# Kernel optimization log

Hardware: AMD Instinct MI355X
Metric: run time of the kernel (lower is better)

## Reference

```python
import jax, jax.numpy as jnp
import numpy as np

N_SRC = 100_000   # hetero[s].num_nodes
N_DST = 100_000   # hetero[d].num_nodes
E     = 800_000   # edge_index.size(1)
D_SRC = 256       # node_dims['src']
D_DST = 256       # node_dims['dst']
D_REL = 128       # d_rel


def setup_inputs() -> dict:
    key = jax.random.key(0)
    ks = jax.random.split(key, 6)
    x_src = jax.random.normal(ks[0], (N_SRC, D_SRC), jnp.float32)
    x_dst = jax.random.normal(ks[1], (N_DST, D_DST), jnp.float32)
    # nn.Linear(d_in, d_rel, bias=False) weights, stored transposed as [d_in, d_rel]
    W_src = jax.random.normal(ks[2], (D_SRC, D_REL), jnp.float32) / np.sqrt(D_SRC).astype(np.float32)
    W_dst = jax.random.normal(ks[3], (D_DST, D_REL), jnp.float32) / np.sqrt(D_DST).astype(np.float32)
    edge_src = jax.random.randint(ks[4], (E,), 0, N_SRC, jnp.int32)  # edge_index[0]
    edge_dst = jax.random.randint(ks[5], (E,), 0, N_DST, jnp.int32)  # edge_index[1]
    return {"x_src": x_src, "x_dst": x_dst, "W_src": W_src, "W_dst": W_dst,
            "edge_src": edge_src, "edge_dst": edge_dst}


def reference(x_src, x_dst, W_src, W_dst, edge_src, edge_dst):
    # Per-type linear projection (bias-free), as in self.proj[nt](feats)
    p_src = x_src @ W_src            # [N_src, d_rel]
    p_dst = x_dst @ W_dst            # projected per module, unused by this edge type
    del p_dst

    # Degree of each destination (A.sum(dim=1)), clamped to >= 1.
    deg = jax.ops.segment_sum(jnp.ones((E,), jnp.float32), edge_dst,
                              num_segments=N_DST)
    deg = jnp.maximum(deg, 1.0)      # [N_dst]

    # Degree-normalized SpMM: sum of source features per destination / deg.
    # (coalescing duplicate edges sums their unit values; segment_sum matches.)
    agg = jax.ops.segment_sum(p_src[edge_src], edge_dst,
                              num_segments=N_DST)            # [N_dst, d_rel]
    dst = agg / deg[:, None]

    # rel_embs[et] = {'dst': dst, 'src_in': x_proj[s], 'deg_dst': deg}
    return dst, p_src, deg
```

## Files before the change

### kernel.cpp

```cpp
#include <hip/hip_runtime.h>
#include <hip/hip_bf16.h>

#define D_SRC 256
#define D_REL 128

typedef __bf16 bf16x8 __attribute__((ext_vector_type(8)));
typedef float f32x4 __attribute__((ext_vector_type(4)));

__global__ void zero_kernel(int* __restrict__ p, int n) {
    int i = blockIdx.x * 256 + threadIdx.x;
    if (i < n) p[i] = 0;
}

__global__ __launch_bounds__(64) void prep_w_kernel(const float* __restrict__ W,
                                                    bf16x8* __restrict__ Wt) {
    int c = blockIdx.x;
    int ks = c >> 3, n = c & 7;
    int lane = threadIdx.x;
    int col = n * 16 + (lane & 15);
    int k0 = ks * 32 + (lane >> 4) * 8;
    bf16x8 v;
#pragma unroll
    for (int j = 0; j < 8; ++j) v[j] = (__bf16)W[(size_t)(k0 + j) * D_REL + col];
    Wt[c * 64 + lane] = v;
}

__global__ __launch_bounds__(512) void proj_mfma_kernel(
    const float* __restrict__ x, const f32x4* __restrict__ Wt,
    float* __restrict__ out, unsigned short* __restrict__ out_bf, int M) {
    __shared__ f32x4 blds[4096];
    int tid = threadIdx.x;
#pragma unroll
    for (int i = 0; i < 8; ++i) blds[tid + i * 512] = Wt[tid + i * 512];

    int wave = tid >> 6, lane = tid & 63;
    int row = blockIdx.x * 128 + wave * 16 + (lane & 15);
    int rowc = min(row, M - 1);
    int kb = lane >> 4;

    f32x4 acc[8];
#pragma unroll
    for (int n = 0; n < 8; ++n) acc[n] = (f32x4)(0.f);

    __syncthreads();

    const float* xr = x + (size_t)rowc * D_SRC + kb * 8;
    const bf16x8* b8 = (const bf16x8*)blds;
#pragma unroll
    for (int ks = 0; ks < 8; ++ks) {
        f32x4 a0 = *(const f32x4*)(xr + ks * 32);
        f32x4 a1 = *(const f32x4*)(xr + ks * 32 + 4);
        bf16x8 af;
        af[0] = (__bf16)a0[0]; af[1] = (__bf16)a0[1];
        af[2] = (__bf16)a0[2]; af[3] = (__bf16)a0[3];
        af[4] = (__bf16)a1[0]; af[5] = (__bf16)a1[1];
        af[6] = (__bf16)a1[2]; af[7] = (__bf16)a1[3];
#pragma unroll
        for (int n = 0; n < 8; ++n) {
            bf16x8 bf = b8[ks * 512 + n * 64 + lane];
            acc[n] = __builtin_amdgcn_mfma_f32_16x16x32_bf16(af, bf, acc[n], 0, 0, 0);
        }
    }

    int orow0 = blockIdx.x * 128 + wave * 16 + (lane >> 4) * 4;
    int ocol = lane & 15;
#pragma unroll
    for (int reg = 0; reg < 4; ++reg) {
        int r = orow0 + reg;
        if (r < M) {
            float* o = out + (size_t)r * D_REL + ocol;
            unsigned short* ob = out_bf + (size_t)r * D_REL + ocol;
#pragma unroll
            for (int n = 0; n < 8; ++n) {
                float v = acc[n][reg];
                o[n * 16] = v;
                ob[n * 16] = (unsigned short)(__bfloat16_as_ushort(__float2bfloat16(v)));
            }
        }
    }
}

__global__ void count_kernel(const int* __restrict__ edge_dst, int* __restrict__ deg_i,
                             int* __restrict__ pos_arr, int E) {
    int e = blockIdx.x * 256 + threadIdx.x;
    if (e < E) pos_arr[e] = atomicAdd(&deg_i[edge_dst[e]], 1);
}

__global__ __launch_bounds__(1024) void scan_blocks(
    const int* __restrict__ deg_i, int* __restrict__ incl,
    int* __restrict__ bsums, int n) {
    int i = blockIdx.x * 1024 + threadIdx.x;
    int v = (i < n) ? deg_i[i] : 0;
    int lane = threadIdx.x & 63;
    int wid = threadIdx.x >> 6;
    int x = v;
#pragma unroll
    for (int off = 1; off < 64; off <<= 1) {
        int y = __shfl_up(x, off, 64);
        if (lane >= off) x += y;
    }
    __shared__ int wsum[16];
    if (lane == 63) wsum[wid] = x;
    __syncthreads();
    if (wid == 0 && lane < 16) {
        int s = wsum[lane];
#pragma unroll
        for (int off = 1; off < 16; off <<= 1) {
            int y = __shfl_up(s, off, 64);
            if (lane >= off) s += y;
        }
        wsum[lane] = s;
    }
    __syncthreads();
    int add = (wid > 0) ? wsum[wid - 1] : 0;
    x += add;
    if (i < n) incl[i] = x;
    if (threadIdx.x == 1023) bsums[blockIdx.x] = x;
}

__global__ __launch_bounds__(128) void scan_sums(int* __restrict__ bs, int nb) {
    __shared__ int tmp[128];
    int t = threadIdx.x;
    int v = (t < nb) ? bs[t] : 0;
    tmp[t] = v;
    __syncthreads();
    for (int off = 1; off < 128; off <<= 1) {
        int y = 0;
        if (t >= off) y = tmp[t - off];
        __syncthreads();
        tmp[t] += y;
        __syncthreads();
    }
    if (t < nb) bs[t] = tmp[t] - v;
}

__global__ __launch_bounds__(1024) void finalize_kernel(
    const int* __restrict__ deg_i, const int* __restrict__ incl,
    const int* __restrict__ bsums, int* __restrict__ row_start,
    float* __restrict__ deg_out, int n, int E) {
    int i = blockIdx.x * 1024 + threadIdx.x;
    if (i < n) {
        int off = bsums[blockIdx.x];
        row_start[i] = off + incl[i] - deg_i[i];
        deg_out[i] = (float)max(deg_i[i], 1);
    }
    if (i == 0) row_start[n] = E;
}

__global__ void fill_kernel(const int* __restrict__ edge_src,
                            const int* __restrict__ edge_dst,
                            const int* __restrict__ row_start,
                            const int* __restrict__ pos_arr,
                            int* __restrict__ bucket, int E) {
    int e = blockIdx.x * 256 + threadIdx.x;
    if (e < E) {
        int d = edge_dst[e];
        bucket[row_start[d] + pos_arr[e]] = edge_src[e];
    }
}

__global__ __launch_bounds__(256) void gather_kernel(
    const unsigned int* __restrict__ p_bf, const int* __restrict__ row_start,
    const int* __restrict__ bucket, const float* __restrict__ deg_out,
    float* __restrict__ dst, int n) {
    int row = blockIdx.x * 4 + (threadIdx.x >> 6);
    int lane = threadIdx.x & 63;
    if (row >= n) return;
    int beg = row_start[row], end = row_start[row + 1];
    float ax = 0.f, ay = 0.f;
    int idx = beg;
    for (; idx + 4 <= end; idx += 4) {
        int s0 = bucket[idx + 0];
        int s1 = bucket[idx + 1];
        int s2 = bucket[idx + 2];
        int s3 = bucket[idx + 3];
        unsigned int v0 = p_bf[(size_t)s0 * 64 + lane];
        unsigned int v1 = p_bf[(size_t)s1 * 64 + lane];
        unsigned int v2 = p_bf[(size_t)s2 * 64 + lane];
        unsigned int v3 = p_bf[(size_t)s3 * 64 + lane];
        ax += __uint_as_float(v0 << 16) + __uint_as_float(v1 << 16)
            + __uint_as_float(v2 << 16) + __uint_as_float(v3 << 16);
        ay += __uint_as_float(v0 & 0xffff0000u) + __uint_as_float(v1 & 0xffff0000u)
            + __uint_as_float(v2 & 0xffff0000u) + __uint_as_float(v3 & 0xffff0000u);
    }
    for (; idx < end; ++idx) {
        int s = bucket[idx];
        unsigned int v = p_bf[(size_t)s * 64 + lane];
        ax += __uint_as_float(v << 16);
        ay += __uint_as_float(v & 0xffff0000u);
    }
    float dinv = 1.0f / deg_out[row];
    float2 o;
    o.x = ax * dinv;
    o.y = ay * dinv;
    ((float2*)dst)[(size_t)row * 64 + lane] = o;
}

extern "C" void kernel_launch(void* const* d_in, const int* in_sizes, int n_in,
                              void* d_out, int out_size, void* d_ws, size_t ws_size,
                              hipStream_t stream) {
    const float* x_src = (const float*)d_in[0];
    const float* W_src = (const float*)d_in[2];
    const int* edge_src = (const int*)d_in[4];
    const int* edge_dst = (const int*)d_in[5];

    const int N_SRC = in_sizes[0] / D_SRC;
    const int N_DST = in_sizes[1] / D_SRC;
    const int E = in_sizes[4];

    float* out_dst = (float*)d_out;
    float* out_psrc = out_dst + (size_t)N_DST * D_REL;
    float* out_deg = out_psrc + (size_t)N_SRC * D_REL;

    int* deg_i = (int*)d_ws;
    int* incl = deg_i + N_DST;
    int* row_start = incl + N_DST;
    int* bsums = row_start + N_DST + 1;
    int* pos_arr = bsums + 128;
    int* bucket = pos_arr + E;
    size_t int_bytes = (size_t)(3 * N_DST + 1 + 128 + 2 * (size_t)E) * sizeof(int);
    size_t wt_off = (int_bytes + 255) & ~(size_t)255;
    bf16x8* Wt = (bf16x8*)((char*)d_ws + wt_off);
    size_t pbf_off = wt_off + 65536;
    unsigned short* p_bf = (unsigned short*)((char*)d_ws + pbf_off);

    zero_kernel<<<(N_DST + 255) / 256, 256, 0, stream>>>(deg_i, N_DST);
    prep_w_kernel<<<64, 64, 0, stream>>>(W_src, Wt);
    proj_mfma_kernel<<<(N_SRC + 127) / 128, 512, 0, stream>>>(
        x_src, (const f32x4*)Wt, out_psrc, p_bf, N_SRC);
    count_kernel<<<(E + 255) / 256, 256, 0, stream>>>(edge_dst, deg_i, pos_arr, E);
    int nb = (N_DST + 1023) / 1024;
    scan_blocks<<<nb, 1024, 0, stream>>>(deg_i, incl, bsums, N_DST);
    scan_sums<<<1, 128, 0, stream>>>(bsums, nb);
    finalize_kernel<<<nb, 1024, 0, stream>>>(deg_i, incl, bsums, row_start, out_deg, N_DST, E);
    fill_kernel<<<(E + 255) / 256, 256, 0, stream>>>(edge_src, edge_dst, row_start, pos_arr, bucket, E);
    gather_kernel<<<(N_DST + 3) / 4, 256, 0, stream>>>(
        (const unsigned int*)p_bf, row_start, bucket, out_deg, out_dst, N_DST);
}
```

Baseline: 146.9 us.

## Switch projection to 32x32x16 MFMA, drop LDS weight staging, prefetch A

The projection GEMM moves from 16x16x32 to 32x32x16 bf16 MFMA tiles, so each wave covers 32 rows with four accumulators, and the weight prep layout is changed to match. The LDS staging of weights and the block barrier are removed; B fragments are read straight from global memory, where the small weight array is expected to stay cache-resident. The next A fragment is software-prefetched, and blocks shrink to 256 threads with an occupancy hint. The output store pattern changes to per-lane 32-column strides, which may coalesce differently.

```diff
diff --git a/kernel.cpp b/kernel.cpp
--- a/kernel.cpp
+++ b/kernel.cpp
@@ -6,6 +6,7 @@
 
 typedef __bf16 bf16x8 __attribute__((ext_vector_type(8)));
 typedef float f32x4 __attribute__((ext_vector_type(4)));
+typedef float f32x16 __attribute__((ext_vector_type(16)));
 
 __global__ void zero_kernel(int* __restrict__ p, int n) {
     int i = blockIdx.x * 256 + threadIdx.x;
@@ -15,66 +16,68 @@
 __global__ __launch_bounds__(64) void prep_w_kernel(const float* __restrict__ W,
                                                     bf16x8* __restrict__ Wt) {
     int c = blockIdx.x;
-    int ks = c >> 3, n = c & 7;
+    int ks = c >> 2, n = c & 3;
     int lane = threadIdx.x;
-    int col = n * 16 + (lane & 15);
-    int k0 = ks * 32 + (lane >> 4) * 8;
+    int col = n * 32 + (lane & 31);
+    int k0 = ks * 16 + (lane >> 5) * 8;
     bf16x8 v;
 #pragma unroll
     for (int j = 0; j < 8; ++j) v[j] = (__bf16)W[(size_t)(k0 + j) * D_REL + col];
     Wt[c * 64 + lane] = v;
 }
 
-__global__ __launch_bounds__(512) void proj_mfma_kernel(
-    const float* __restrict__ x, const f32x4* __restrict__ Wt,
+__global__ __launch_bounds__(256, 4) void proj_mfma_kernel(
+    const float* __restrict__ x, const bf16x8* __restrict__ Wt,
     float* __restrict__ out, unsigned short* __restrict__ out_bf, int M) {
-    __shared__ f32x4 blds[4096];
     int tid = threadIdx.x;
-#pragma unroll
-    for (int i = 0; i < 8; ++i) blds[tid + i * 512] = Wt[tid + i * 512];
-
     int wave = tid >> 6, lane = tid & 63;
-    int row = blockIdx.x * 128 + wave * 16 + (lane & 15);
+    int half = lane >> 5;
+    int r31 = lane & 31;
+    int row = blockIdx.x * 128 + wave * 32 + r31;
     int rowc = min(row, M - 1);
-    int kb = lane >> 4;
-
-    f32x4 acc[8];
-#pragma unroll
-    for (int n = 0; n < 8; ++n) acc[n] = (f32x4)(0.f);
-
-    __syncthreads();
-
-    const float* xr = x + (size_t)rowc * D_SRC + kb * 8;
-    const bf16x8* b8 = (const bf16x8*)blds;
-#pragma unroll
-    for (int ks = 0; ks < 8; ++ks) {
-        f32x4 a0 = *(const f32x4*)(xr + ks * 32);
-        f32x4 a1 = *(const f32x4*)(xr + ks * 32 + 4);
+    const float* xr = x + (size_t)rowc * D_SRC + half * 8;
+
+    f32x16 acc[4];
+#pragma unroll
+    for (int n = 0; n < 4; ++n) acc[n] = (f32x16)(0.f);
+
+    f32x4 a0 = *(const f32x4*)(xr);
+    f32x4 a1 = *(const f32x4*)(xr + 4);
+
+#pragma unroll
+    for (int ks = 0; ks < 16; ++ks) {
+        bf16x8 b0 = Wt[(ks * 4 + 0) * 64 + lane];
+        bf16x8 b1 = Wt[(ks * 4 + 1) * 64 + lane];
+        bf16x8 b2 = Wt[(ks * 4 + 2) * 64 + lane];
+        bf16x8 b3 = Wt[(ks * 4 + 3) * 64 + lane];
+        f32x4 na0, na1;
+        if (ks < 15) {
+            na0 = *(const f32x4*)(xr + (ks + 1) * 16);
+            na1 = *(const f32x4*)(xr + (ks + 1) * 16 + 4);
+        }
         bf16x8 af;
         af[0] = (__bf16)a0[0]; af[1] = (__bf16)a0[1];
         af[2] = (__bf16)a0[2]; af[3] = (__bf16)a0[3];
         af[4] = (__bf16)a1[0]; af[5] = (__bf16)a1[1];
         af[6] = (__bf16)a1[2]; af[7] = (__bf16)a1[3];
-#pragma unroll
-        for (int n = 0; n < 8; ++n) {
-            bf16x8 bf = b8[ks * 512 + n * 64 + lane];
-            acc[n] = __builtin_amdgcn_mfma_f32_16x16x32_bf16(af, bf, acc[n], 0, 0, 0);
-        }
-    }
-
-    int orow0 = blockIdx.x * 128 + wave * 16 + (lane >> 4) * 4;
-    int ocol = lane & 15;
-#pragma unroll
-    for (int reg = 0; reg < 4; ++reg) {
-        int r = orow0 + reg;
-        if (r < M) {
-            float* o = out + (size_t)r * D_REL + ocol;
-            unsigned short* ob = out_bf + (size_t)r * D_REL + ocol;
-#pragma unroll
-            for (int n = 0; n < 8; ++n) {
+        acc[0] = __builtin_amdgcn_mfma_f32_32x32x16_bf16(af, b0, acc[0], 0, 0, 0);
+        acc[1] = __builtin_amdgcn_mfma_f32_32x32x16_bf16(af, b1, acc[1], 0, 0, 0);
+        acc[2] = __builtin_amdgcn_mfma_f32_32x32x16_bf16(af, b2, acc[2], 0, 0, 0);
+        acc[3] = __builtin_amdgcn_mfma_f32_32x32x16_bf16(af, b3, acc[3], 0, 0, 0);
+        if (ks < 15) { a0 = na0; a1 = na1; }
+    }
+
+    int rbase = blockIdx.x * 128 + wave * 32 + 4 * half;
+#pragma unroll
+    for (int n = 0; n < 4; ++n) {
+#pragma unroll
+        for (int reg = 0; reg < 16; ++reg) {
+            int r = rbase + (reg & 3) + 8 * (reg >> 2);
+            if (r < M) {
                 float v = acc[n][reg];
-                o[n * 16] = v;
-                ob[n * 16] = (unsigned short)(__bfloat16_as_ushort(__float2bfloat16(v)));
+                size_t o = (size_t)r * D_REL + n * 32 + r31;
+                out[o] = v;
+                out_bf[o] = __bfloat16_as_ushort(__float2bfloat16(v));
             }
         }
     }
@@ -226,8 +229,8 @@
 
     zero_kernel<<<(N_DST + 255) / 256, 256, 0, stream>>>(deg_i, N_DST);
     prep_w_kernel<<<64, 64, 0, stream>>>(W_src, Wt);
-    proj_mfma_kernel<<<(N_SRC + 127) / 128, 512, 0, stream>>>(
-        x_src, (const f32x4*)Wt, out_psrc, p_bf, N_SRC);
+    proj_mfma_kernel<<<(N_SRC + 127) / 128, 256, 0, stream>>>(
+        x_src, Wt, out_psrc, p_bf, N_SRC);
     count_kernel<<<(E + 255) / 256, 256, 0, stream>>>(edge_dst, deg_i, pos_arr, E);
     int nb = (N_DST + 1023) / 1024;
     scan_blocks<<<nb, 1024, 0, stream>>>(deg_i, incl, bsums, N_DST);
```

Measured after the change: 153.6 us. 1.05x slower.

## Drop LDS weight staging in projection; split N across waves and prefetch A

Applied to the files above, without the earlier changes.

The projection kernel no longer copies the 64KB bf16 weight tile into shared memory per block. Weights are read directly from global/L2, and each wave now computes 16 rows by 64 columns, so two waves share a row tile. All A-row loads are issued up front into registers to overlap memory latency. This removes the per-block LDS fill and barrier and raises occupancy, at the cost of redundant A reads across wave pairs and more global/L2 traffic for weights.

```diff
diff --git a/kernel.cpp b/kernel.cpp
--- a/kernel.cpp
+++ b/kernel.cpp
@@ -25,56 +25,58 @@
     Wt[c * 64 + lane] = v;
 }
 
-__global__ __launch_bounds__(512) void proj_mfma_kernel(
-    const float* __restrict__ x, const f32x4* __restrict__ Wt,
+__global__ __launch_bounds__(256, 4) void proj_mfma_kernel(
+    const float* __restrict__ x, const bf16x8* __restrict__ Wt,
     float* __restrict__ out, unsigned short* __restrict__ out_bf, int M) {
-    __shared__ f32x4 blds[4096];
     int tid = threadIdx.x;
-#pragma unroll
-    for (int i = 0; i < 8; ++i) blds[tid + i * 512] = Wt[tid + i * 512];
-
     int wave = tid >> 6, lane = tid & 63;
-    int row = blockIdx.x * 128 + wave * 16 + (lane & 15);
-    int rowc = min(row, M - 1);
-    int kb = lane >> 4;
-
-    f32x4 acc[8];
-#pragma unroll
-    for (int n = 0; n < 8; ++n) acc[n] = (f32x4)(0.f);
-
-    __syncthreads();
-
+    int row0 = blockIdx.x * 32 + (wave >> 1) * 16;
+    int n0 = (wave & 1) * 4;
+    int r15 = lane & 15, kb = lane >> 4;
+
+    int rowc = min(row0 + r15, M - 1);
     const float* xr = x + (size_t)rowc * D_SRC + kb * 8;
-    const bf16x8* b8 = (const bf16x8*)blds;
+
+    f32x4 a[16];
+#pragma unroll
+    for (int i = 0; i < 8; ++i) {
+        a[2 * i + 0] = *(const f32x4*)(xr + i * 32);
+        a[2 * i + 1] = *(const f32x4*)(xr + i * 32 + 4);
+    }
+
+    f32x4 acc[4];
+#pragma unroll
+    for (int n = 0; n < 4; ++n) acc[n] = (f32x4)(0.f);
+
 #pragma unroll
     for (int ks = 0; ks < 8; ++ks) {
-        f32x4 a0 = *(const f32x4*)(xr + ks * 32);
-        f32x4 a1 = *(const f32x4*)(xr + ks * 32 + 4);
+        bf16x8 b0 = Wt[(ks * 8 + n0 + 0) * 64 + lane];
+        bf16x8 b1 = Wt[(ks * 8 + n0 + 1) * 64 + lane];
+        bf16x8 b2 = Wt[(ks * 8 + n0 + 2) * 64 + lane];
+        bf16x8 b3 = Wt[(ks * 8 + n0 + 3) * 64 + lane];
+        f32x4 a0 = a[2 * ks], a1 = a[2 * ks + 1];
         bf16x8 af;
         af[0] = (__bf16)a0[0]; af[1] = (__bf16)a0[1];
         af[2] = (__bf16)a0[2]; af[3] = (__bf16)a0[3];
         af[4] = (__bf16)a1[0]; af[5] = (__bf16)a1[1];
         af[6] = (__bf16)a1[2]; af[7] = (__bf16)a1[3];
-#pragma unroll
-        for (int n = 0; n < 8; ++n) {
-            bf16x8 bf = b8[ks * 512 + n * 64 + lane];
-            acc[n] = __builtin_amdgcn_mfma_f32_16x16x32_bf16(af, bf, acc[n], 0, 0, 0);
-        }
-    }
-
-    int orow0 = blockIdx.x * 128 + wave * 16 + (lane >> 4) * 4;
-    int ocol = lane & 15;
+        acc[0] = __builtin_amdgcn_mfma_f32_16x16x32_bf16(af, b0, acc[0], 0, 0, 0);
+        acc[1] = __builtin_amdgcn_mfma_f32_16x16x32_bf16(af, b1, acc[1], 0, 0, 0);
+        acc[2] = __builtin_amdgcn_mfma_f32_16x16x32_bf16(af, b2, acc[2], 0, 0, 0);
+        acc[3] = __builtin_amdgcn_mfma_f32_16x16x32_bf16(af, b3, acc[3], 0, 0, 0);
+    }
+
+    int rbase = row0 + kb * 4;
 #pragma unroll
     for (int reg = 0; reg < 4; ++reg) {
-        int r = orow0 + reg;
+        int r = rbase + reg;
         if (r < M) {
-            float* o = out + (size_t)r * D_REL + ocol;
-            unsigned short* ob = out_bf + (size_t)r * D_REL + ocol;
-#pragma unroll
-            for (int n = 0; n < 8; ++n) {
+            size_t o = (size_t)r * D_REL + n0 * 16 + r15;
+#pragma unroll
+            for (int n = 0; n < 4; ++n) {
                 float v = acc[n][reg];
-                o[n * 16] = v;
-                ob[n * 16] = (unsigned short)(__bfloat16_as_ushort(__float2bfloat16(v)));
+                out[o + n * 16] = v;
+                out_bf[o + n * 16] = __bfloat16_as_ushort(__float2bfloat16(v));
             }
         }
     }
@@ -226,8 +228,8 @@
 
     zero_kernel<<<(N_DST + 255) / 256, 256, 0, stream>>>(deg_i, N_DST);
     prep_w_kernel<<<64, 64, 0, stream>>>(W_src, Wt);
-    proj_mfma_kernel<<<(N_SRC + 127) / 128, 512, 0, stream>>>(
-        x_src, (const f32x4*)Wt, out_psrc, p_bf, N_SRC);
+    proj_mfma_kernel<<<(N_SRC + 31) / 32, 256, 0, stream>>>(
+        x_src, Wt, out_psrc, p_bf, N_SRC);
     count_kernel<<<(E + 255) / 256, 256, 0, stream>>>(edge_dst, deg_i, pos_arr, E);
     int nb = (N_DST + 1023) / 1024;
     scan_blocks<<<nb, 1024, 0, stream>>>(deg_i, incl, bsums, N_DST);
```

Result: slower. 159.0 us (+8.2%).

## Restructure projection GEMM: stage x via direct-to-LDS loads, keep W in registers

Applied to the files above, without the earlier changes.

The projection kernel now handles 32 rows per 256-thread block. It stages the x tile into LDS with global_load_lds and an XOR-swizzled layout, and each wave keeps its 32-column slice of bf16 W in registers instead of loading all of W into LDS per block. The MFMA operands are swapped (W as A, x as B), so the output is transposed per lane and can be written with vectorized f32x4/ushort4 stores instead of scalar ones. This aims to cut the per-block LDS traffic for W and the uncoalesced scalar stores. The cost is more blocks, each re-reading W from global/L2, and higher register pressure.

```diff
diff --git a/kernel.cpp b/kernel.cpp
--- a/kernel.cpp
+++ b/kernel.cpp
@@ -6,6 +6,9 @@
 
 typedef __bf16 bf16x8 __attribute__((ext_vector_type(8)));
 typedef float f32x4 __attribute__((ext_vector_type(4)));
+
+typedef const __attribute__((address_space(1))) void GASV;
+typedef __attribute__((address_space(3))) void LASV;
 
 __global__ void zero_kernel(int* __restrict__ p, int n) {
     int i = blockIdx.x * 256 + threadIdx.x;
@@ -25,57 +28,84 @@
     Wt[c * 64 + lane] = v;
 }
 
-__global__ __launch_bounds__(512) void proj_mfma_kernel(
+__global__ __launch_bounds__(256, 4) void proj_mfma_kernel(
     const float* __restrict__ x, const f32x4* __restrict__ Wt,
     float* __restrict__ out, unsigned short* __restrict__ out_bf, int M) {
-    __shared__ f32x4 blds[4096];
+    __shared__ float xlds[32 * 256];
     int tid = threadIdx.x;
-#pragma unroll
-    for (int i = 0; i < 8; ++i) blds[tid + i * 512] = Wt[tid + i * 512];
-
-    int wave = tid >> 6, lane = tid & 63;
-    int row = blockIdx.x * 128 + wave * 16 + (lane & 15);
-    int rowc = min(row, M - 1);
-    int kb = lane >> 4;
-
-    f32x4 acc[8];
-#pragma unroll
-    for (int n = 0; n < 8; ++n) acc[n] = (f32x4)(0.f);
-
-    __syncthreads();
-
-    const float* xr = x + (size_t)rowc * D_SRC + kb * 8;
-    const bf16x8* b8 = (const bf16x8*)blds;
+    int wid = tid >> 6, lane = tid & 63;
+    int r = lane & 15, kq = lane >> 4;
+    int row0 = blockIdx.x * 32;
+
+#pragma unroll
+    for (int j = 0; j < 8; ++j) {
+        int rl = wid * 8 + j;
+        int grow = min(row0 + rl, M - 1);
+        const float* src = x + (size_t)grow * D_SRC + ((lane ^ j) << 2);
+        __builtin_amdgcn_global_load_lds((GASV*)src, (LASV*)&xlds[rl * 256], 16, 0, 0);
+    }
+
+    f32x4 wfv[2][8];
+#pragma unroll
+    for (int s = 0; s < 2; ++s)
+#pragma unroll
+        for (int ks = 0; ks < 8; ++ks)
+            wfv[s][ks] = Wt[(ks * 8 + wid * 2 + s) * 64 + lane];
+#pragma unroll
+    for (int s = 0; s < 2; ++s)
+#pragma unroll
+        for (int ks = 0; ks < 8; ++ks)
+            asm volatile("" : "+v"(wfv[s][ks]));
+
+    __syncthreads();
+
+    f32x4 acc[2][2];
+#pragma unroll
+    for (int t = 0; t < 2; ++t)
+#pragma unroll
+        for (int s = 0; s < 2; ++s) acc[t][s] = (f32x4)(0.f);
+
+    const f32x4* xl = (const f32x4*)xlds;
+    int r8 = r & 7;
 #pragma unroll
     for (int ks = 0; ks < 8; ++ks) {
-        f32x4 a0 = *(const f32x4*)(xr + ks * 32);
-        f32x4 a1 = *(const f32x4*)(xr + ks * 32 + 4);
-        bf16x8 af;
-        af[0] = (__bf16)a0[0]; af[1] = (__bf16)a0[1];
-        af[2] = (__bf16)a0[2]; af[3] = (__bf16)a0[3];
-        af[4] = (__bf16)a1[0]; af[5] = (__bf16)a1[1];
-        af[6] = (__bf16)a1[2]; af[7] = (__bf16)a1[3];
-#pragma unroll
-        for (int n = 0; n < 8; ++n) {
-            bf16x8 bf = b8[ks * 512 + n * 64 + lane];
-            acc[n] = __builtin_amdgcn_mfma_f32_16x16x32_bf16(af, bf, acc[n], 0, 0, 0);
+        int q0 = ks * 8 + kq * 2;
+#pragma unroll
+        for (int t = 0; t < 2; ++t) {
+            int rl = t * 16 + r;
+            f32x4 a0 = xl[rl * 64 + (q0 ^ r8)];
+            f32x4 a1 = xl[rl * 64 + ((q0 + 1) ^ r8)];
+            bf16x8 xf;
+            xf[0] = (__bf16)a0[0]; xf[1] = (__bf16)a0[1];
+            xf[2] = (__bf16)a0[2]; xf[3] = (__bf16)a0[3];
+            xf[4] = (__bf16)a1[0]; xf[5] = (__bf16)a1[1];
+            xf[6] = (__bf16)a1[2]; xf[7] = (__bf16)a1[3];
+            acc[t][0] = __builtin_amdgcn_mfma_f32_16x16x32_bf16(
+                __builtin_bit_cast(bf16x8, wfv[0][ks]), xf, acc[t][0], 0, 0, 0);
+            acc[t][1] = __builtin_amdgcn_mfma_f32_16x16x32_bf16(
+                __builtin_bit_cast(bf16x8, wfv[1][ks]), xf, acc[t][1], 0, 0, 0);
         }
     }
 
-    int orow0 = blockIdx.x * 128 + wave * 16 + (lane >> 4) * 4;
-    int ocol = lane & 15;
-#pragma unroll
-    for (int reg = 0; reg < 4; ++reg) {
-        int r = orow0 + reg;
-        if (r < M) {
-            float* o = out + (size_t)r * D_REL + ocol;
-            unsigned short* ob = out_bf + (size_t)r * D_REL + ocol;
-#pragma unroll
-            for (int n = 0; n < 8; ++n) {
-                float v = acc[n][reg];
-                o[n * 16] = v;
-                ob[n * 16] = (unsigned short)(__bfloat16_as_ushort(__float2bfloat16(v)));
-            }
+    int col0 = wid * 32;
+#pragma unroll
+    for (int t = 0; t < 2; ++t) {
+        int prow = row0 + t * 16 + r;
+        if (prow < M) {
+            size_t o0 = (size_t)prow * D_REL + col0 + kq * 4;
+            *(f32x4*)(out + o0) = acc[t][0];
+            *(f32x4*)(out + o0 + 16) = acc[t][1];
+            ushort4 b0, b1;
+            b0.x = __bfloat16_as_ushort(__float2bfloat16(acc[t][0][0]));
+            b0.y = __bfloat16_as_ushort(__float2bfloat16(acc[t][0][1]));
+            b0.z = __bfloat16_as_ushort(__float2bfloat16(acc[t][0][2]));
+            b0.w = __bfloat16_as_ushort(__float2bfloat16(acc[t][0][3]));
+            b1.x = __bfloat16_as_ushort(__float2bfloat16(acc[t][1][0]));
+            b1.y = __bfloat16_as_ushort(__float2bfloat16(acc[t][1][1]));
+            b1.z = __bfloat16_as_ushort(__float2bfloat16(acc[t][1][2]));
+            b1.w = __bfloat16_as_ushort(__float2bfloat16(acc[t][1][3]));
+            *(ushort4*)(out_bf + o0) = b0;
+            *(ushort4*)(out_bf + o0 + 16) = b1;
         }
     }
 }
@@ -226,7 +256,7 @@
 
     zero_kernel<<<(N_DST + 255) / 256, 256, 0, stream>>>(deg_i, N_DST);
     prep_w_kernel<<<64, 64, 0, stream>>>(W_src, Wt);
-    proj_mfma_kernel<<<(N_SRC + 127) / 128, 512, 0, stream>>>(
+    proj_mfma_kernel<<<(N_SRC + 31) / 32, 256, 0, stream>>>(
         x_src, (const f32x4*)Wt, out_psrc, p_bf, N_SRC);
     count_kernel<<<(E + 255) / 256, 256, 0, stream>>>(edge_dst, deg_i, pos_arr, E);
     int nb = (N_DST + 1023) / 1024;
```

Result: no change. 146.5 us (-0.3%).
